# Performance work log

Hardware: AMD Instinct MI355X
Metric: run time of the kernel (lower is better)

## Reference

```python
import jax, jax.numpy as jnp
import numpy as np

EMB, KEY, HEAD, CTX = 1024, 64, 64, 4096
B, T = 4, 4096

def setup_inputs() -> dict:
    key = jax.random.key(0)
    ks = jax.random.split(key, 4)
    s = 1.0 / np.sqrt(EMB)
    return {
        "embeddings": jax.random.normal(ks[0], (B, T, EMB), dtype=jnp.float32),
        "Wk": jax.random.normal(ks[1], (EMB, KEY), dtype=jnp.float32) * s,
        "bk": jnp.zeros((KEY,), dtype=jnp.float32),
        "Wq": jax.random.normal(ks[2], (EMB, KEY), dtype=jnp.float32) * s,
        "bq": jnp.zeros((KEY,), dtype=jnp.float32),
        "Wv": jax.random.normal(ks[3], (EMB, HEAD), dtype=jnp.float32) * s,
        "bv": jnp.zeros((HEAD,), dtype=jnp.float32),
    }

def reference(embeddings, Wk, bk, Wq, bq, Wv, bv):
    # Linear projections: [B, T, E] @ [E, D] -> [B, T, D]
    keys = embeddings @ Wk + bk
    queries = embeddings @ Wq + bq
    values = embeddings @ Wv + bv
    # Scores: [B, T, T]
    scores = jnp.einsum("btd,bsd->bts", queries, keys) / jnp.sqrt(jnp.float32(KEY))
    t = scores.shape[1]
    # causal mask: -inf strictly above diagonal
    causal = jnp.tril(jnp.ones((t, t), dtype=bool))
    scores = jnp.where(causal, scores, -jnp.inf)
    weights = jax.nn.softmax(scores, axis=-1)
    return jnp.einsum("bts,bsh->bth", weights, values)
```

## Files before the change

### kernel.cpp

```cpp
#include <hip/hip_runtime.h>
#include <hip/hip_bf16.h>

#define EMB 1024
#define NB  4
#define TT  4096
#define DD  64

static constexpr float SCALE2 = 0.125f * 1.4426950408889634f;

typedef __bf16          bfrag    __attribute__((ext_vector_type(8)));
typedef float           f32x4    __attribute__((ext_vector_type(4)));
typedef unsigned short  ushort8t __attribute__((ext_vector_type(8)));
typedef unsigned short  ushort4t __attribute__((ext_vector_type(4)));
typedef unsigned int    uint32;

__device__ __forceinline__ unsigned short f2bf(float f) {
    __hip_bfloat16 h = __float2bfloat16(f);
    return __builtin_bit_cast(unsigned short, h);
}
__device__ __forceinline__ float bf2f(unsigned short u) {
    uint32 v = ((uint32)u) << 16;
    return __builtin_bit_cast(float, v);
}
__device__ __forceinline__ uint32 pk2(float a, float b) {
    return (uint32)f2bf(a) | ((uint32)f2bf(b) << 16);
}

__global__ __launch_bounds__(256) void prep_wt(
    const float* __restrict__ Wk, const float* __restrict__ Wq,
    const float* __restrict__ Wv, unsigned short* __restrict__ Wt)
{
    const int o = blockIdx.x * 256 + threadIdx.x;
    const int n = o >> 10, k = o & 1023;
    float v;
    if (n < 64)       v = Wk[k * 64 + n];
    else if (n < 128) v = Wq[k * 64 + (n - 64)] * SCALE2;
    else              v = Wv[k * 64 + (n - 128)];
    Wt[o] = f2bf(v);
}

#define PSTR 66

__global__ __launch_bounds__(256) void qkv_mfma(
    const float* __restrict__ emb,
    const unsigned short* __restrict__ Wt,
    const float* __restrict__ bk, const float* __restrict__ bq,
    const float* __restrict__ bv,
    unsigned short* __restrict__ Qb, unsigned short* __restrict__ Kb,
    unsigned short* __restrict__ Vt)
{
    __shared__ unsigned short elds[64 * PSTR];
    __shared__ unsigned short wlds[192 * PSTR];

    const int tid = threadIdx.x;
    const int w = tid >> 6, l = tid & 63;
    const int lr = l & 15, lg = l >> 4;
    const int m0 = blockIdx.x * 64;

    f32x4 acc[12];
#pragma unroll
    for (int i = 0; i < 12; ++i) acc[i] = (f32x4){0.f, 0.f, 0.f, 0.f};

    const int er = tid >> 2, ec = (tid & 3) * 16;

    float4 f0, f1, f2, f3;
    ushort8t wr[6];
    {
        const float* src = emb + (size_t)(m0 + er) * EMB + ec;
        f0 = *(const float4*)(src + 0);
        f1 = *(const float4*)(src + 4);
        f2 = *(const float4*)(src + 8);
        f3 = *(const float4*)(src + 12);
#pragma unroll
        for (int i = 0; i < 6; ++i) {
            const int idx = tid + i * 256;
            const int row = idx >> 3, c = (idx & 7) * 8;
            wr[i] = *(const ushort8t*)&Wt[(size_t)row * 1024 + c];
        }
    }

    for (int it = 0; it < 16; ++it) {
        __syncthreads();
        {
            ushort8t lo, hi;
            lo[0]=f2bf(f0.x); lo[1]=f2bf(f0.y); lo[2]=f2bf(f0.z); lo[3]=f2bf(f0.w);
            lo[4]=f2bf(f1.x); lo[5]=f2bf(f1.y); lo[6]=f2bf(f1.z); lo[7]=f2bf(f1.w);
            hi[0]=f2bf(f2.x); hi[1]=f2bf(f2.y); hi[2]=f2bf(f2.z); hi[3]=f2bf(f2.w);
            hi[4]=f2bf(f3.x); hi[5]=f2bf(f3.y); hi[6]=f2bf(f3.z); hi[7]=f2bf(f3.w);
            *(ushort8t*)&elds[er * PSTR + ec]     = lo;
            *(ushort8t*)&elds[er * PSTR + ec + 8] = hi;
#pragma unroll
            for (int i = 0; i < 6; ++i) {
                const int idx = tid + i * 256;
                const int row = idx >> 3, c = (idx & 7) * 8;
                *(ushort8t*)&wlds[row * PSTR + c] = wr[i];
            }
        }
        if (it < 15) {
            const int kn = (it + 1) * 64;
            const float* src = emb + (size_t)(m0 + er) * EMB + kn + ec;
            f0 = *(const float4*)(src + 0);
            f1 = *(const float4*)(src + 4);
            f2 = *(const float4*)(src + 8);
            f3 = *(const float4*)(src + 12);
#pragma unroll
            for (int i = 0; i < 6; ++i) {
                const int idx = tid + i * 256;
                const int row = idx >> 3, c = (idx & 7) * 8;
                wr[i] = *(const ushort8t*)&Wt[(size_t)row * 1024 + kn + c];
            }
        }
        __syncthreads();
#pragma unroll
        for (int c = 0; c < 2; ++c) {
            bfrag a = *(const bfrag*)&elds[(w * 16 + lr) * PSTR + c * 32 + lg * 8];
#pragma unroll
            for (int nt = 0; nt < 12; ++nt) {
                bfrag bb = *(const bfrag*)&wlds[(nt * 16 + lr) * PSTR + c * 32 + lg * 8];
                acc[nt] = __builtin_amdgcn_mfma_f32_16x16x32_bf16(a, bb, acc[nt], 0, 0, 0);
            }
        }
    }

    const int rbase = m0 + w * 16 + lg * 4;
#pragma unroll
    for (int nt = 0; nt < 12; ++nt) {
        const int n = nt * 16 + lr;
        float bias;
        if (n < 64)       bias = bk[n];
        else if (n < 128) bias = bq[n - 64] * SCALE2;
        else              bias = bv[n - 128];
        if (nt < 8) {
            unsigned short* dst = (nt < 4) ? Kb : Qb;
            const int d = (nt < 4) ? n : (n - 64);
#pragma unroll
            for (int rg = 0; rg < 4; ++rg)
                dst[(size_t)(rbase + rg) * 64 + d] = f2bf(acc[nt][rg] + bias);
        } else {
            const int h = n - 128;
            const int b = rbase >> 12, t = rbase & (TT - 1);
            ushort4t pk;
#pragma unroll
            for (int rg = 0; rg < 4; ++rg) pk[rg] = f2bf(acc[nt][rg] + bias);
            *(ushort4t*)&Vt[((size_t)b * 64 + h) * TT + t] = pk;
        }
    }
}

#define PST 66

__global__ __launch_bounds__(64) void attn_part(
    const unsigned short* __restrict__ Qb,
    const unsigned short* __restrict__ Kb,
    const unsigned short* __restrict__ Vt,
    unsigned short* __restrict__ po, float* __restrict__ pml,
    int chunk, int nch)
{
    __shared__ unsigned short plds[32 * PST];

    const int idx  = blockIdx.x;
    const int c    = idx >> 9;
    const int b    = idx & 3;
    const int ti32 = 127 - ((idx >> 2) & 127);
    const int nkt  = (ti32 >> 1) + 1;
    const int kt0  = c * chunk;
    if (kt0 >= nkt) return;
    const int kt1 = min(nkt, kt0 + chunk);

    const int l  = threadIdx.x;
    const int lr = l & 15, g = l >> 4;
    const int q0 = ti32 * 32;
    const size_t bTT = (size_t)b * TT;

    bfrag qa[2][2];
#pragma unroll
    for (int s = 0; s < 2; ++s) {
        const size_t qr = (bTT + q0 + s * 16 + lr) * 64 + g * 8;
        qa[s][0] = *(const bfrag*)&Qb[qr];
        qa[s][1] = *(const bfrag*)&Qb[qr + 32];
    }

    f32x4 o[2][4];
#pragma unroll
    for (int s = 0; s < 2; ++s)
#pragma unroll
        for (int ht = 0; ht < 4; ++ht) o[s][ht] = (f32x4){0.f, 0.f, 0.f, 0.f};
    float mrow[2] = {-1e30f, -1e30f};
    float lrow[2] = {0.f, 0.f};

    for (int kt = kt0; kt < kt1; ++kt) {
        const int k0 = kt * 64;

        bfrag kf[4][2];
#pragma unroll
        for (int nt = 0; nt < 4; ++nt) {
            const size_t kr = (bTT + k0 + nt * 16 + lr) * 64 + g * 8;
            kf[nt][0] = *(const bfrag*)&Kb[kr];
            kf[nt][1] = *(const bfrag*)&Kb[kr + 32];
        }
        bfrag vf[4][2];
#pragma unroll
        for (int ht = 0; ht < 4; ++ht) {
            const size_t vr = ((size_t)b * 64 + ht * 16 + lr) * TT + k0 + g * 8;
            vf[ht][0] = *(const bfrag*)&Vt[vr];
            vf[ht][1] = *(const bfrag*)&Vt[vr + 32];
        }
        const bool diag = (kt == nkt - 1);

#pragma unroll
        for (int s = 0; s < 2; ++s) {
            f32x4 sv[4];
#pragma unroll
            for (int nt = 0; nt < 4; ++nt) {
                sv[nt] = (f32x4){0.f, 0.f, 0.f, 0.f};
                sv[nt] = __builtin_amdgcn_mfma_f32_16x16x32_bf16(kf[nt][0], qa[s][0], sv[nt], 0, 0, 0);
                sv[nt] = __builtin_amdgcn_mfma_f32_16x16x32_bf16(kf[nt][1], qa[s][1], sv[nt], 0, 0, 0);
            }
            const int qrow = q0 + s * 16 + lr;
            if (diag) {
#pragma unroll
                for (int nt = 0; nt < 4; ++nt)
#pragma unroll
                    for (int rg = 0; rg < 4; ++rg) {
                        const int key = k0 + nt * 16 + 4 * g + rg;
                        if (key > qrow) sv[nt][rg] = -1e30f;
                    }
            }
            float pm = sv[0][0];
#pragma unroll
            for (int nt = 0; nt < 4; ++nt)
#pragma unroll
                for (int rg = 0; rg < 4; ++rg) pm = fmaxf(pm, sv[nt][rg]);
            pm = fmaxf(pm, __shfl_xor(pm, 16));
            pm = fmaxf(pm, __shfl_xor(pm, 32));

            if (!__all(pm - mrow[s] <= 8.0f)) {
                const float nm = fmaxf(mrow[s], pm);
                const float cr = exp2f(mrow[s] - nm);
                mrow[s] = nm;
                lrow[s] *= cr;
#pragma unroll
                for (int ht = 0; ht < 4; ++ht) o[s][ht] *= cr;
            }

            float ls = 0.f;
            uint32 pw[8];
#pragma unroll
            for (int nt = 0; nt < 4; ++nt)
#pragma unroll
                for (int h = 0; h < 2; ++h) {
                    const float pa_ = exp2f(sv[nt][2 * h]     - mrow[s]);
                    const float pb_ = exp2f(sv[nt][2 * h + 1] - mrow[s]);
                    ls += pa_ + pb_;
                    pw[nt * 2 + h] = pk2(pa_, pb_);
                }
            ls += __shfl_xor(ls, 16);
            ls += __shfl_xor(ls, 32);
            lrow[s] += ls;

            const int prow = (s * 16 + lr) * PST;
#pragma unroll
            for (int nt = 0; nt < 4; ++nt)
#pragma unroll
                for (int h = 0; h < 2; ++h)
                    *(uint32*)&plds[prow + nt * 16 + 4 * g + 2 * h] = pw[nt * 2 + h];

#pragma unroll
            for (int cc = 0; cc < 2; ++cc) {
                bfrag pa = *(const bfrag*)&plds[prow + cc * 32 + g * 8];
#pragma unroll
                for (int ht = 0; ht < 4; ++ht)
                    o[s][ht] = __builtin_amdgcn_mfma_f32_16x16x32_bf16(pa, vf[ht][cc], o[s][ht], 0, 0, 0);
            }
        }
    }

    const int slot = (((b << 7) + ti32) * nch) + c;
    const size_t pob = (size_t)slot * 2048;
#pragma unroll
    for (int s = 0; s < 2; ++s)
#pragma unroll
        for (int ht = 0; ht < 4; ++ht)
#pragma unroll
            for (int rg = 0; rg < 4; ++rg)
                po[pob + (size_t)(((s * 4 + ht) * 4 + rg) * 64 + l)] = f2bf(o[s][ht][rg]);
    if (g == 0) {
#pragma unroll
        for (int s = 0; s < 2; ++s) {
            pml[slot * 64 + s * 16 + lr]      = mrow[s];
            pml[slot * 64 + 32 + s * 16 + lr] = lrow[s];
        }
    }
}

__global__ __launch_bounds__(256) void attn_merge(
    const unsigned short* __restrict__ po, const float* __restrict__ pml,
    float* __restrict__ out, int chunk, int nch)
{
    const int idx  = blockIdx.x;
    const int b    = idx & 3;
    const int ti32 = idx >> 2;
    const int nkt  = (ti32 >> 1) + 1;
    const int nc   = (nkt + chunk - 1) / chunk;

    const int e0   = threadIdx.x * 8;
    const int lane = e0 & 63;
    const int rg   = (e0 >> 6) & 3;
    const int ht   = (e0 >> 8) & 3;
    const int s    = e0 >> 10;
    const int row  = s * 16 + ((lane >> 4) << 2) + rg;
    const int col0 = ht * 16 + (lane & 15);
    const int slot0 = ((b << 7) + ti32) * nch;

    float M = -1e30f;
    for (int c = 0; c < nc; ++c)
        M = fmaxf(M, pml[(slot0 + c) * 64 + row]);

    float den = 0.f;
    float acc[8];
#pragma unroll
    for (int i = 0; i < 8; ++i) acc[i] = 0.f;

    for (int c = 0; c < nc; ++c) {
        const float wgt = exp2f(pml[(slot0 + c) * 64 + row] - M);
        den += wgt * pml[(slot0 + c) * 64 + 32 + row];
        const ushort8t v = *(const ushort8t*)&po[(size_t)(slot0 + c) * 2048 + e0];
#pragma unroll
        for (int j = 0; j < 8; ++j) acc[j] += wgt * bf2f(v[j]);
    }
    const float inv = 1.0f / den;
    float* dst = out + ((size_t)b * TT + ti32 * 32 + row) * 64 + col0;
    float4 o0 = {acc[0] * inv, acc[1] * inv, acc[2] * inv, acc[3] * inv};
    float4 o1 = {acc[4] * inv, acc[5] * inv, acc[6] * inv, acc[7] * inv};
    *(float4*)(dst)     = o0;
    *(float4*)(dst + 4) = o1;
}

extern "C" void kernel_launch(void* const* d_in, const int* in_sizes, int n_in,
                              void* d_out, int out_size, void* d_ws, size_t ws_size,
                              hipStream_t stream)
{
    const float* emb = (const float*)d_in[0];
    const float* Wk  = (const float*)d_in[1];
    const float* bk  = (const float*)d_in[2];
    const float* Wq  = (const float*)d_in[3];
    const float* bq  = (const float*)d_in[4];
    const float* Wv  = (const float*)d_in[5];
    const float* bv  = (const float*)d_in[6];
    float* out = (float*)d_out;

    char* base = (char*)d_ws;
    unsigned short* Qb = (unsigned short*)(base);
    unsigned short* Kb = (unsigned short*)(base + (2u << 20));
    unsigned short* Vt = (unsigned short*)(base + (4u << 20));
    unsigned short* Wt = (unsigned short*)(base + (6u << 20));
    const size_t pbase = ((size_t)6 << 20) + (512u << 10);

    int nch = 8;
    for (;;) {
        const size_t need = pbase +
            (size_t)512 * nch * (2048 * sizeof(unsigned short) + 64 * sizeof(float));
        if (need <= ws_size || nch == 1) break;
        nch >>= 1;
    }
    const int chunk = 64 / nch;
    unsigned short* po = (unsigned short*)(base + pbase);
    float* pml = (float*)(po + (size_t)512 * nch * 2048);

    prep_wt<<<192 * 1024 / 256, 256, 0, stream>>>(Wk, Wq, Wv, Wt);
    qkv_mfma<<<(NB * TT) / 64, 256, 0, stream>>>(emb, Wt, bk, bq, bv, Qb, Kb, Vt);
    attn_part<<<512 * nch, 64, 0, stream>>>(Qb, Kb, Vt, po, pml, chunk, nch);
    attn_merge<<<512, 256, 0, stream>>>(po, pml, out, chunk, nch);
}
```

Baseline: 85.85 us.

## Replace LDS P-matrix staging with ds_bpermute register shuffles in attention

Removes the shared-memory round trip that turned the softmax probabilities from MFMA output layout into A-operand layout, using ds_bpermute cross-lane shuffles selected by lane group instead. It also switches K/V loads to incrementing pointers instead of recomputing addresses, uses a tree max reduction, and sets a min-blocks-per-CU launch bound. The aim is lower LDS traffic, fewer address computations and higher occupancy, at the cost of more bpermute instructions (16 per chunk, half discarded) and possible register pressure from the occupancy bound.

```diff
diff --git a/kernel.cpp b/kernel.cpp
--- a/kernel.cpp
+++ b/kernel.cpp
@@ -13,6 +13,7 @@
 typedef unsigned short  ushort8t __attribute__((ext_vector_type(8)));
 typedef unsigned short  ushort4t __attribute__((ext_vector_type(4)));
 typedef unsigned int    uint32;
+typedef uint32          uint32x4 __attribute__((ext_vector_type(4)));
 
 __device__ __forceinline__ unsigned short f2bf(float f) {
     __hip_bfloat16 h = __float2bfloat16(f);
@@ -147,17 +148,13 @@
     }
 }
 
-#define PST 66
-
-__global__ __launch_bounds__(64) void attn_part(
+__global__ __launch_bounds__(64, 4) void attn_part(
     const unsigned short* __restrict__ Qb,
     const unsigned short* __restrict__ Kb,
     const unsigned short* __restrict__ Vt,
     unsigned short* __restrict__ po, float* __restrict__ pml,
     int chunk, int nch)
 {
-    __shared__ unsigned short plds[32 * PST];
-
     const int idx  = blockIdx.x;
     const int c    = idx >> 9;
     const int b    = idx & 3;
@@ -180,6 +177,17 @@
         qa[s][1] = *(const bfrag*)&Qb[qr + 32];
     }
 
+    const unsigned short* kpA = Kb + (bTT + (size_t)kt0 * 64 + lr) * 64 + g * 8;
+    const unsigned short* kpB = kpA + 2048;
+    const unsigned short* vp0 = Vt + ((size_t)b * 64 +  0 + lr) * TT + (size_t)kt0 * 64 + g * 8;
+    const unsigned short* vp1 = vp0 + 16 * TT;
+    const unsigned short* vp2 = vp0 + 32 * TT;
+    const unsigned short* vp3 = vp0 + 48 * TT;
+
+    const int addr_a = (lr + 32 * (g & 1)) * 4;
+    const int addr_b = addr_a + 64;
+    const bool ghi = (g >= 2);
+
     f32x4 o[2][4];
 #pragma unroll
     for (int s = 0; s < 2; ++s)
@@ -189,23 +197,23 @@
     float lrow[2] = {0.f, 0.f};
 
     for (int kt = kt0; kt < kt1; ++kt) {
-        const int k0 = kt * 64;
-
         bfrag kf[4][2];
-#pragma unroll
-        for (int nt = 0; nt < 4; ++nt) {
-            const size_t kr = (bTT + k0 + nt * 16 + lr) * 64 + g * 8;
-            kf[nt][0] = *(const bfrag*)&Kb[kr];
-            kf[nt][1] = *(const bfrag*)&Kb[kr + 32];
-        }
+        kf[0][0] = *(const bfrag*)(kpA +    0);
+        kf[0][1] = *(const bfrag*)(kpA +   32);
+        kf[1][0] = *(const bfrag*)(kpA + 1024);
+        kf[1][1] = *(const bfrag*)(kpA + 1056);
+        kf[2][0] = *(const bfrag*)(kpB +    0);
+        kf[2][1] = *(const bfrag*)(kpB +   32);
+        kf[3][0] = *(const bfrag*)(kpB + 1024);
+        kf[3][1] = *(const bfrag*)(kpB + 1056);
         bfrag vf[4][2];
-#pragma unroll
-        for (int ht = 0; ht < 4; ++ht) {
-            const size_t vr = ((size_t)b * 64 + ht * 16 + lr) * TT + k0 + g * 8;
-            vf[ht][0] = *(const bfrag*)&Vt[vr];
-            vf[ht][1] = *(const bfrag*)&Vt[vr + 32];
-        }
+        vf[0][0] = *(const bfrag*)(vp0);  vf[0][1] = *(const bfrag*)(vp0 + 32);
+        vf[1][0] = *(const bfrag*)(vp1);  vf[1][1] = *(const bfrag*)(vp1 + 32);
+        vf[2][0] = *(const bfrag*)(vp2);  vf[2][1] = *(const bfrag*)(vp2 + 32);
+        vf[3][0] = *(const bfrag*)(vp3);  vf[3][1] = *(const bfrag*)(vp3 + 32);
+
         const bool diag = (kt == nkt - 1);
+        const int  k0   = kt * 64;
 
 #pragma unroll
         for (int s = 0; s < 2; ++s) {
@@ -226,11 +234,10 @@
                         if (key > qrow) sv[nt][rg] = -1e30f;
                     }
             }
-            float pm = sv[0][0];
-#pragma unroll
-            for (int nt = 0; nt < 4; ++nt)
-#pragma unroll
-                for (int rg = 0; rg < 4; ++rg) pm = fmaxf(pm, sv[nt][rg]);
+            float pm = fmaxf(fmaxf(fmaxf(sv[0][0], sv[0][1]), fmaxf(sv[0][2], sv[0][3])),
+                             fmaxf(fmaxf(sv[1][0], sv[1][1]), fmaxf(sv[1][2], sv[1][3])));
+            pm = fmaxf(pm, fmaxf(fmaxf(fmaxf(sv[2][0], sv[2][1]), fmaxf(sv[2][2], sv[2][3])),
+                                 fmaxf(fmaxf(sv[3][0], sv[3][1]), fmaxf(sv[3][2], sv[3][3]))));
             pm = fmaxf(pm, __shfl_xor(pm, 16));
             pm = fmaxf(pm, __shfl_xor(pm, 32));
 
@@ -258,21 +265,27 @@
             ls += __shfl_xor(ls, 32);
             lrow[s] += ls;
 
-            const int prow = (s * 16 + lr) * PST;
-#pragma unroll
-            for (int nt = 0; nt < 4; ++nt)
-#pragma unroll
-                for (int h = 0; h < 2; ++h)
-                    *(uint32*)&plds[prow + nt * 16 + 4 * g + 2 * h] = pw[nt * 2 + h];
-
 #pragma unroll
             for (int cc = 0; cc < 2; ++cc) {
-                bfrag pa = *(const bfrag*)&plds[prow + cc * 32 + g * 8];
-#pragma unroll
-                for (int ht = 0; ht < 4; ++ht)
-                    o[s][ht] = __builtin_amdgcn_mfma_f32_16x16x32_bf16(pa, vf[ht][cc], o[s][ht], 0, 0, 0);
-            }
-        }
+                uint32x4 dw;
+#pragma unroll
+                for (int w2 = 0; w2 < 4; ++w2) {
+                    const int addr = (w2 < 2) ? addr_a : addr_b;
+                    const uint32 lo = (uint32)__builtin_amdgcn_ds_bpermute(
+                        addr, (int)pw[4 * cc + (w2 & 1)]);
+                    const uint32 hi = (uint32)__builtin_amdgcn_ds_bpermute(
+                        addr, (int)pw[4 * cc + 2 + (w2 & 1)]);
+                    dw[w2] = ghi ? hi : lo;
+                }
+                const bfrag pa = __builtin_bit_cast(bfrag, dw);
+                o[s][0] = __builtin_amdgcn_mfma_f32_16x16x32_bf16(pa, vf[0][cc], o[s][0], 0, 0, 0);
+                o[s][1] = __builtin_amdgcn_mfma_f32_16x16x32_bf16(pa, vf[1][cc], o[s][1], 0, 0, 0);
+                o[s][2] = __builtin_amdgcn_mfma_f32_16x16x32_bf16(pa, vf[2][cc], o[s][2], 0, 0, 0);
+                o[s][3] = __builtin_amdgcn_mfma_f32_16x16x32_bf16(pa, vf[3][cc], o[s][3], 0, 0, 0);
+            }
+        }
+        kpA += 4096; kpB += 4096;
+        vp0 += 64; vp1 += 64; vp2 += 64; vp3 += 64;
     }
 
     const int slot = (((b << 7) + ti32) * nch) + c;
```

After: 128.3 us. 1.49x slower.
